# Kernel tuning notes

Hardware: AMD Instinct MI355X
Metric: run time of the kernel (lower is better)

The kernel has to match this reference:

```python
import jax, jax.numpy as jnp
import numpy as np

N = 100000      # nodes
E = 1600000     # edges (avg degree 16)
DIM = 128
HEADS = 8
HEAD_DIM = DIM // HEADS


def setup_inputs() -> dict:
    key = jax.random.key(0)
    k = jax.random.split(key, 6)
    stdv = 1.0 / np.sqrt(HEAD_DIM)  # init scale from reset_parameters
    x = jax.random.normal(k[0], (N, DIM), dtype=jnp.float32)
    edge_index = jax.random.randint(k[1], (2, E), 0, N, dtype=jnp.int32)
    W = jax.random.uniform(k[2], (DIM, DIM), jnp.float32, -stdv, stdv)
    b_proj = jnp.zeros((DIM,), jnp.float32)
    att_src = jax.random.uniform(k[3], (1, HEADS, HEAD_DIM), jnp.float32, -stdv, stdv)
    att_dst = jax.random.uniform(k[4], (1, HEADS, HEAD_DIM), jnp.float32, -stdv, stdv)
    bias = jnp.zeros((DIM,), jnp.float32)
    return {"x": x, "edge_index": edge_index, "W": W, "b_proj": b_proj,
            "att_src": att_src, "att_dst": att_dst, "bias": bias}


def reference(x, edge_index, W, b_proj, att_src, att_dst, bias):
    n = x.shape[0]
    # project, split heads: [N, H, Hd]
    xh = (x @ W.T + b_proj).reshape(n, HEADS, HEAD_DIM)
    # add_remaining_self_loops (random edges assumed loop-free)
    loops = jnp.arange(n, dtype=edge_index.dtype)
    src = jnp.concatenate([edge_index[0], loops])  # x_j index
    dst = jnp.concatenate([edge_index[1], loops])  # aggregation index
    # per-node attention logits [N, H]
    a_src = jnp.einsum('nhd,hd->nh', xh, att_src[0])
    a_dst = jnp.einsum('nhd,hd->nh', xh, att_dst[0])
    # per-edge score [Etot, H]
    alpha = jax.nn.leaky_relu(a_src[src] + a_dst[dst], negative_slope=0.2)
    # segment softmax over edges grouped by destination (self loops => no empty segments)
    mx = jax.ops.segment_max(alpha, dst, num_segments=n)
    ex = jnp.exp(alpha - mx[dst])
    denom = jax.ops.segment_sum(ex, dst, num_segments=n)
    alpha = ex / denom[dst]
    # message = alpha * x_j, scatter-add to destination
    msg = alpha[:, :, None] * xh[src]                      # [Etot, H, Hd]
    out = jax.ops.segment_sum(msg, dst, num_segments=n)    # [N, H, Hd]
    return out.reshape(n, DIM) + bias
```

## Files before the change

### kernel.cpp

```cpp
#include <hip/hip_runtime.h>
#include <hip/hip_bf16.h>

typedef __hip_bfloat16 bf16;
typedef __hip_bfloat162 bf162;
typedef __attribute__((ext_vector_type(8))) short short8;
typedef __attribute__((ext_vector_type(4))) float f32x4;

#define NN 100000
#define NE 1600000
#define ETOT (NE + NN)
#define DIM 128
#define HEADS 8

#define BSH 9
#define NBUK ((NN + 511) >> BSH)
#define EPB 2048
#define B1 ((ETOT + EPB - 1) / EPB)
#define MAXPER 40
#define PROJ_BLKS ((NN + 63) / 64)

__device__ __forceinline__ float lrelu(float v) { return v > 0.f ? v : 0.2f * v; }

__device__ __forceinline__ float load1(const void* p, int i, int isbf) {
    return isbf ? __bfloat162float(((const bf16*)p)[i]) : ((const float*)p)[i];
}
__device__ __forceinline__ float2 load2(const void* p, size_t pairIdx, int isbf) {
    if (isbf) return __bfloat1622float2(((const bf162*)p)[pairIdx]);
    return ((const float2*)p)[pairIdx];
}
__device__ __forceinline__ short f2bf(float f) {
    bf16 h = __float2bfloat16(f);
    return *reinterpret_cast<short*>(&h);
}

__global__ __launch_bounds__(256) void aug_kernel(
    const void* __restrict__ W, const void* __restrict__ bproj,
    const void* __restrict__ atts, const void* __restrict__ attd,
    int* __restrict__ flag, bf16* __restrict__ waug, float* __restrict__ wc)
{
    __shared__ bf16 Wl[128 * 128];
    __shared__ float av[256];
    __shared__ float red[256];
    const int tid = threadIdx.x;

    {
        const bf16* wb = (const bf16*)W;
        float m = 0.f;
        for (int i = tid; i < 8192; i += 256) {
            float v = fabsf(__bfloat162float(wb[i]));
            if (!(v < 1e30f)) v = 1e30f;
            m = fmaxf(m, v);
        }
        red[tid] = m;
        __syncthreads();
        for (int s = 128; s > 0; s >>= 1) {
            if (tid < s) red[tid] = fmaxf(red[tid], red[tid + s]);
            __syncthreads();
        }
    }
    const int isbf = (red[0] < 1.0f) ? 1 : 0;
    if (tid == 0) *flag = isbf;

    for (int i = tid; i < 2048; i += 256) {
        short8 v;
        if (isbf) {
            v = ((const short8*)W)[i];
        } else {
            const float* wp = (const float*)W + (size_t)i * 8;
            #pragma unroll
            for (int j = 0; j < 8; ++j) v[j] = f2bf(wp[j]);
        }
        ((short8*)Wl)[i] = v;
    }
    av[tid & 255] = (tid < 128) ? load1(atts, tid, isbf)
                                : load1(attd, tid - 128, isbf);
    __syncthreads();

    #pragma unroll
    for (int it = 0; it < 8; ++it) {
        const int o = tid + it * 256;
        const int row = o >> 7, col = o & 127;
        const int h = row & 7;
        const int ao = (row < 8) ? 0 : 128;
        float s = 0.f;
        #pragma unroll
        for (int t = 0; t < 16; ++t)
            s += av[ao + h * 16 + t] * __bfloat162float(Wl[(h * 16 + t) * 128 + col]);
        waug[o] = __float2bfloat16(s);
    }
    if (tid < 16) {
        const int h = tid & 7;
        const int ao = (tid < 8) ? 0 : 128;
        float s = 0.f;
        #pragma unroll
        for (int t = 0; t < 16; ++t)
            s += load1(bproj, h * 16 + t, isbf) * av[ao + h * 16 + t];
        wc[tid] = s;
    }
}

__global__ __launch_bounds__(256) void projcount_kernel(
    const void* __restrict__ x, const void* __restrict__ W,
    const void* __restrict__ bproj, const bf16* __restrict__ waug,
    const float* __restrict__ wc, const int* __restrict__ flag,
    bf16* __restrict__ xh, float* __restrict__ asrc, float* __restrict__ adst,
    const int* __restrict__ ei, int* __restrict__ cntmat)
{
    __shared__ short8 Wf[2304];
    __shared__ float bsh[DIM], csh[16];

    const int tid = threadIdx.x;

    if (blockIdx.x >= PROJ_BLKS) {
        const int b = blockIdx.x - PROJ_BLKS;
        int* cnt = (int*)Wf;
        for (int i = tid; i < NBUK; i += 256) cnt[i] = 0;
        __syncthreads();
        const int base = b * EPB;
        #pragma unroll
        for (int it = 0; it < EPB / 1024; ++it) {
            const int e = base + it * 1024 + tid * 4;
            if (e < ETOT) {
                int4 d4;
                if (e < NE) {
                    d4 = *(const int4*)(ei + NE + e);
                } else {
                    d4.x = e - NE; d4.y = d4.x + 1; d4.z = d4.x + 2; d4.w = d4.x + 3;
                }
                atomicAdd(&cnt[d4.x >> BSH], 1);
                atomicAdd(&cnt[d4.y >> BSH], 1);
                atomicAdd(&cnt[d4.z >> BSH], 1);
                atomicAdd(&cnt[d4.w >> BSH], 1);
            }
        }
        __syncthreads();
        for (int k = tid; k < NBUK; k += 256) cntmat[k * B1 + b] = cnt[k];
        return;
    }

    const int isbf = *flag;

    for (int c = tid; c < 2048; c += 256) {
        int j = c >> 4, kc = c & 15;
        int kb = kc >> 2, quad = kc & 3;
        int lane = quad * 16 + (j & 15);
        int jt = j >> 4;
        short8 v;
        if (isbf) {
            v = ((const short8*)W)[c];
        } else {
            const float* wp = (const float*)W + (size_t)j * DIM + kc * 8;
            #pragma unroll
            for (int i = 0; i < 8; ++i) v[i] = f2bf(wp[i]);
        }
        Wf[(jt * 4 + kb) * 64 + lane] = v;
    }
    {
        int c = tid;
        if (c < 256) {
            int j2 = c >> 4, kc = c & 15;
            int kb = kc >> 2, quad = kc & 3;
            Wf[(32 + kb) * 64 + quad * 16 + j2] = ((const short8*)waug)[c];
        }
    }
    if (tid < DIM) bsh[tid] = load1(bproj, tid, isbf);
    if (tid < 16)  csh[tid] = wc[tid];
    __syncthreads();

    const int w = tid >> 6;
    const int l = tid & 63;
    const int quad = l >> 4, mr = l & 15;
    const int n0 = blockIdx.x * 64 + w * 16;
    const int nArd = min(n0 + mr, NN - 1);

    short8 afr[4];
    if (isbf) {
        const short8* xp = (const short8*)x + (size_t)nArd * 16;
        #pragma unroll
        for (int kb = 0; kb < 4; ++kb) afr[kb] = xp[kb * 4 + quad];
    } else {
        const float* xp = (const float*)x + (size_t)nArd * DIM;
        #pragma unroll
        for (int kb = 0; kb < 4; ++kb) {
            const float* cp = xp + kb * 32 + quad * 8;
            float4 c0 = *(const float4*)cp;
            float4 c1 = *(const float4*)(cp + 4);
            short8 v;
            v[0] = f2bf(c0.x); v[1] = f2bf(c0.y); v[2] = f2bf(c0.z); v[3] = f2bf(c0.w);
            v[4] = f2bf(c1.x); v[5] = f2bf(c1.y); v[6] = f2bf(c1.z); v[7] = f2bf(c1.w);
            afr[kb] = v;
        }
    }

    f32x4 accs[8];
    #pragma unroll
    for (int jt = 0; jt < 8; ++jt) {
        f32x4 acc = {0.f, 0.f, 0.f, 0.f};
        #pragma unroll
        for (int kb = 0; kb < 4; ++kb) {
            short8 b = Wf[(jt * 4 + kb) * 64 + l];
            acc = __builtin_amdgcn_mfma_f32_16x16x32_bf16(afr[kb], b, acc, 0, 0, 0);
        }
        accs[jt] = acc;
    }
    f32x4 acca = {0.f, 0.f, 0.f, 0.f};
    #pragma unroll
    for (int kb = 0; kb < 4; ++kb) {
        short8 b = Wf[(32 + kb) * 64 + l];
        acca = __builtin_amdgcn_mfma_f32_16x16x32_bf16(afr[kb], b, acca, 0, 0, 0);
    }

    __syncthreads();

    bf16* sw = ((bf16*)Wf) + w * (16 * 136);
    #pragma unroll
    for (int jt = 0; jt < 8; ++jt) {
        const int jj = jt * 16 + mr;
        const float bv = bsh[jj];
        #pragma unroll
        for (int r = 0; r < 4; ++r)
            sw[(quad * 4 + r) * 136 + jj] = __float2bfloat16(accs[jt][r] + bv);
    }
    #pragma unroll
    for (int g = 0; g < 4; ++g) {
        const int row = g * 4 + (l >> 4);
        const int n = n0 + row;
        if (n < NN)
            *((short8*)(xh + (size_t)n * DIM) + (l & 15)) =
                *(const short8*)(sw + row * 136 + (l & 15) * 8);
    }

    {
        const float cst = csh[mr];
        #pragma unroll
        for (int r = 0; r < 4; ++r) {
            const int n = n0 + quad * 4 + r;
            if (n < NN) {
                float v = acca[r] + cst;
                if (mr < 8) asrc[n * HEADS + mr] = v;
                else        adst[n * HEADS + (mr - 8)] = v;
            }
        }
    }
}

__global__ __launch_bounds__(256) void csr_colscan_kernel(const int* __restrict__ cntmat,
                                                          int* __restrict__ cntpre,
                                                          int* __restrict__ btot)
{
    const int k = blockIdx.x, t = threadIdx.x;
    int v[4];
    int s = 0;
    #pragma unroll
    for (int j = 0; j < 4; ++j) {
        const int c = t * 4 + j;
        v[j] = (c < B1) ? cntmat[k * B1 + c] : 0;
        s += v[j];
    }
    const int l = t & 63, w = t >> 6;
    int inc = s;
    #pragma unroll
    for (int off = 1; off < 64; off <<= 1) {
        int u = __shfl_up(inc, off);
        if (l >= off) inc += u;
    }
    __shared__ int wt[4];
    if (l == 63) wt[w] = inc;
    __syncthreads();
    int add = 0;
    #pragma unroll
    for (int i = 0; i < 4; ++i) if (i < w) add += wt[i];
    int run = add + inc - s;
    #pragma unroll
    for (int j = 0; j < 4; ++j) {
        const int c = t * 4 + j;
        if (c < B1) cntpre[k * B1 + c] = run;
        run += v[j];
    }
    if (t == 255) btot[k] = add + inc;
}

__device__ __forceinline__ void scan_btot(const int* __restrict__ btot,
                                          int* __restrict__ bb, int* __restrict__ wt4)
{
    const int t = threadIdx.x;
    const int v = (t < NBUK) ? btot[t] : 0;
    const int l = t & 63, w = t >> 6;
    int inc = v;
    #pragma unroll
    for (int off = 1; off < 64; off <<= 1) {
        int u = __shfl_up(inc, off);
        if (l >= off) inc += u;
    }
    if (l == 63) wt4[w] = inc;
    __syncthreads();
    int add = 0;
    #pragma unroll
    for (int i = 0; i < 4; ++i) if (i < w) add += wt4[i];
    if (t < NBUK) bb[t] = add + inc - v;
    __syncthreads();
}

__global__ __launch_bounds__(256) void csr_scatter_kernel(const int* __restrict__ ei,
                                                          const int* __restrict__ cntpre,
                                                          const int* __restrict__ btot,
                                                          int* __restrict__ esrc)
{
    __shared__ int cur[NBUK];
    __shared__ int bb[NBUK];
    __shared__ int wt4[4];
    const int t = threadIdx.x, b = blockIdx.x;

    scan_btot(btot, bb, wt4);
    for (int k = t; k < NBUK; k += 256) cur[k] = bb[k] + cntpre[k * B1 + b];
    __syncthreads();

    const int base = b * EPB;
    #pragma unroll
    for (int it = 0; it < EPB / 1024; ++it) {
        const int e = base + it * 1024 + t * 4;
        if (e < ETOT) {
            int4 d4, s4;
            if (e < NE) {
                s4 = *(const int4*)(ei + e);
                d4 = *(const int4*)(ei + NE + e);
            } else {
                s4.x = e - NE; s4.y = s4.x + 1; s4.z = s4.x + 2; s4.w = s4.x + 3;
                d4 = s4;
            }
            const int p0 = atomicAdd(&cur[d4.x >> BSH], 1);
            const int p1 = atomicAdd(&cur[d4.y >> BSH], 1);
            const int p2 = atomicAdd(&cur[d4.z >> BSH], 1);
            const int p3 = atomicAdd(&cur[d4.w >> BSH], 1);
            esrc[p0] = s4.x | ((d4.x & 511) << 17);
            esrc[p1] = s4.y | ((d4.y & 511) << 17);
            esrc[p2] = s4.z | ((d4.z & 511) << 17);
            esrc[p3] = s4.w | ((d4.w & 511) << 17);
        }
    }
}

__global__ __launch_bounds__(256) void csr_bucket_kernel(const int* __restrict__ btot,
                                                         int* __restrict__ esrc,
                                                         int* __restrict__ rowstart)
{
    __shared__ int hist[512];
    __shared__ int pre[512];
    __shared__ int bb[NBUK];
    __shared__ int wt4[4];
    const int k = blockIdx.x, t = threadIdx.x;

    scan_btot(btot, bb, wt4);
    const int start = bb[k];
    const int end = start + btot[k];
    if (k == 0 && t == 0) rowstart[NN] = ETOT;

    hist[t] = 0;
    hist[t + 256] = 0;
    __syncthreads();

    int v[MAXPER];
    #pragma unroll
    for (int j = 0; j < MAXPER; ++j) {
        const int idx = start + j * 256 + t;
        v[j] = (idx < end) ? esrc[idx] : -1;
    }
    #pragma unroll
    for (int j = 0; j < MAXPER; ++j)
        if (v[j] >= 0) atomicAdd(&hist[(v[j] >> 17) & 511], 1);
    __syncthreads();

    const int h0 = hist[2 * t], h1 = hist[2 * t + 1];
    const int pv = h0 + h1;
    const int l = t & 63, w = t >> 6;
    int inc = pv;
    #pragma unroll
    for (int off = 1; off < 64; off <<= 1) {
        int u = __shfl_up(inc, off);
        if (l >= off) inc += u;
    }
    if (l == 63) wt4[w] = inc;
    __syncthreads();
    int add = 0;
    #pragma unroll
    for (int i = 0; i < 4; ++i) if (i < w) add += wt4[i];
    const int ex = add + inc - pv;
    pre[2 * t] = ex;
    pre[2 * t + 1] = ex + h0;

    const int d0 = (k << BSH) + 2 * t;
    if (d0 < NN)     rowstart[d0]     = start + ex;
    if (d0 + 1 < NN) rowstart[d0 + 1] = start + ex + h0;
    __syncthreads();

    #pragma unroll
    for (int j = 0; j < MAXPER; ++j) {
        if (v[j] >= 0) {
            const int pos = atomicAdd(&pre[(v[j] >> 17) & 511], 1);
            esrc[start + pos] = v[j] & 0x1FFFF;
        }
    }
}

__global__ __launch_bounds__(256) void gather_kernel(
    const int* __restrict__ rowstart, const int* __restrict__ esrc,
    const float* __restrict__ asrc, const float* __restrict__ adst,
    const bf16* __restrict__ xh, const void* __restrict__ bias,
    const int* __restrict__ flag, void* __restrict__ out)
{
    const int d = blockIdx.x * 4 + (threadIdx.x >> 6);
    if (d >= NN) return;
    const int l = threadIdx.x & 63;
    const int h = l >> 3;
    const int isbf = *flag;

    const float ad = adst[d * HEADS + h];
    const int r0 = rowstart[d], r1 = rowstart[d + 1];
    const bf162* __restrict__ xrow = (const bf162*)xh;
    float a0 = 0.f, a1 = 0.f, ds = 0.f;

    int p = r0;
    for (; p + 8 <= r1; p += 8) {
        int s[8];
        #pragma unroll
        for (int j = 0; j < 8; ++j) s[j] = esrc[p + j];
        float v[8];
        #pragma unroll
        for (int j = 0; j < 8; ++j) v[j] = asrc[(unsigned)s[j] * HEADS + h];
        float2 xv[8];
        #pragma unroll
        for (int j = 0; j < 8; ++j)
            xv[j] = __bfloat1622float2(xrow[(unsigned)s[j] * 64u + (unsigned)l]);
        #pragma unroll
        for (int j = 0; j < 8; ++j) {
            float wj = __expf(lrelu(v[j] + ad));
            a0 += wj * xv[j].x;
            a1 += wj * xv[j].y;
            ds += wj;
        }
    }
    for (; p + 4 <= r1; p += 4) {
        int s0 = esrc[p + 0], s1 = esrc[p + 1], s2 = esrc[p + 2], s3 = esrc[p + 3];
        float v0 = asrc[(unsigned)s0 * HEADS + h];
        float v1 = asrc[(unsigned)s1 * HEADS + h];
        float v2 = asrc[(unsigned)s2 * HEADS + h];
        float v3 = asrc[(unsigned)s3 * HEADS + h];
        float2 x0 = __bfloat1622float2(xrow[(unsigned)s0 * 64u + (unsigned)l]);
        float2 x1 = __bfloat1622float2(xrow[(unsigned)s1 * 64u + (unsigned)l]);
        float2 x2 = __bfloat1622float2(xrow[(unsigned)s2 * 64u + (unsigned)l]);
        float2 x3 = __bfloat1622float2(xrow[(unsigned)s3 * 64u + (unsigned)l]);
        float w0 = __expf(lrelu(v0 + ad));
        float w1 = __expf(lrelu(v1 + ad));
        float w2 = __expf(lrelu(v2 + ad));
        float w3 = __expf(lrelu(v3 + ad));
        a0 += w0 * x0.x + w1 * x1.x + w2 * x2.x + w3 * x3.x;
        a1 += w0 * x0.y + w1 * x1.y + w2 * x2.y + w3 * x3.y;
        ds += (w0 + w1) + (w2 + w3);
    }
    for (; p < r1; ++p) {
        int s = esrc[p];
        float w = __expf(lrelu(asrc[(unsigned)s * HEADS + h] + ad));
        float2 xf = __bfloat1622float2(xrow[(unsigned)s * 64u + (unsigned)l]);
        a0 += w * xf.x;
        a1 += w * xf.y;
        ds += w;
    }

    float inv = 1.f / ds;
    float2 bf = load2(bias, l, isbf);
    float o0 = a0 * inv + bf.x;
    float o1 = a1 * inv + bf.y;
    if (isbf) {
        bf162 o;
        o.x = __float2bfloat16(o0);
        o.y = __float2bfloat16(o1);
        ((bf162*)out)[(size_t)d * 64 + l] = o;
    } else {
        ((float2*)out)[(size_t)d * 64 + l] = make_float2(o0, o1);
    }
}

extern "C" void kernel_launch(void* const* d_in, const int* in_sizes, int n_in,
                              void* d_out, int out_size, void* d_ws, size_t ws_size,
                              hipStream_t stream)
{
    const void* x     = d_in[0];
    const int*  ei    = (const int*)d_in[1];
    const void* W     = d_in[2];
    const void* bproj = d_in[3];
    const void* atts  = d_in[4];
    const void* attd  = d_in[5];
    const void* bias  = d_in[6];

    char* p = (char*)d_ws;
    int*    flag     = (int*)p;    p += 16;
    bf16*   xh       = (bf16*)p;   p += (size_t)NN * DIM * sizeof(bf16);
    float*  asrc     = (float*)p;  p += (size_t)NN * HEADS * sizeof(float);
    float*  adst     = (float*)p;  p += (size_t)NN * HEADS * sizeof(float);
    int*    rowstart = (int*)p;    p += (size_t)(NN + 1) * sizeof(int) + 12;
    int*    esrc     = (int*)p;    p += (size_t)ETOT * sizeof(int);
    int*    cntmat   = (int*)p;    p += (size_t)NBUK * B1 * sizeof(int);
    int*    cntpre   = (int*)p;    p += (size_t)NBUK * B1 * sizeof(int);
    int*    btot     = (int*)p;    p += ((NBUK + 3) & ~3) * sizeof(int);
    bf16*   waug     = (bf16*)p;   p += 16 * 128 * sizeof(bf16);
    float*  wc       = (float*)p;  p += 16 * sizeof(float);

    aug_kernel<<<1, 256, 0, stream>>>(W, bproj, atts, attd, flag, waug, wc);
    projcount_kernel<<<PROJ_BLKS + B1, 256, 0, stream>>>(x, W, bproj, waug, wc,
                                                         flag, xh, asrc, adst,
                                                         ei, cntmat);
    csr_colscan_kernel<<<NBUK, 256, 0, stream>>>(cntmat, cntpre, btot);
    csr_scatter_kernel<<<B1, 256, 0, stream>>>(ei, cntpre, btot, esrc);
    csr_bucket_kernel<<<NBUK, 256, 0, stream>>>(btot, esrc, rowstart);
    gather_kernel<<<(NN + 3) / 4, 256, 0, stream>>>(rowstart, esrc, asrc, adst,
                                                    xh, bias, flag, d_out);
}
```

Baseline: 274.9 us.

## Replace per-block count matrix and column scan with global atomic bucket offsets

The bucket-count pass now accumulates per-bucket totals straight into a global array with atomics, and it runs inside the weight-augmentation launch. The scatter blocks, fused with projection, each claim a contiguous slice within each bucket through a global atomic cursor, so the count-matrix write, the column-scan kernel and a separate scatter launch all go away. This cuts two kernel launches and a round trip through the count matrix. In exchange, the order of edges within a bucket is no longer deterministic, and a memset is added to clear the counters.

```diff
diff --git a/kernel.cpp b/kernel.cpp
--- a/kernel.cpp
+++ b/kernel.cpp
@@ -16,6 +16,8 @@
 #define NBUK ((NN + 511) >> BSH)
 #define EPB 2048
 #define B1 ((ETOT + EPB - 1) / EPB)
+#define EPB2 8192
+#define B2 ((ETOT + EPB2 - 1) / EPB2)
 #define MAXPER 40
 #define PROJ_BLKS ((NN + 63) / 64)
 
@@ -33,92 +35,43 @@
     return *reinterpret_cast<short*>(&h);
 }
 
-__global__ __launch_bounds__(256) void aug_kernel(
+__device__ __forceinline__ void scan_btot(const int* __restrict__ btot,
+                                          int* __restrict__ bb, int* __restrict__ wt4)
+{
+    const int t = threadIdx.x;
+    const int v = (t < NBUK) ? btot[t] : 0;
+    const int l = t & 63, w = t >> 6;
+    int inc = v;
+    #pragma unroll
+    for (int off = 1; off < 64; off <<= 1) {
+        int u = __shfl_up(inc, off);
+        if (l >= off) inc += u;
+    }
+    if (l == 63) wt4[w] = inc;
+    __syncthreads();
+    int add = 0;
+    #pragma unroll
+    for (int i = 0; i < 4; ++i) if (i < w) add += wt4[i];
+    if (t < NBUK) bb[t] = add + inc - v;
+    __syncthreads();
+}
+
+__global__ __launch_bounds__(256) void aug_count_kernel(
     const void* __restrict__ W, const void* __restrict__ bproj,
     const void* __restrict__ atts, const void* __restrict__ attd,
-    int* __restrict__ flag, bf16* __restrict__ waug, float* __restrict__ wc)
+    int* __restrict__ flag, bf16* __restrict__ waug, float* __restrict__ wc,
+    const int* __restrict__ ei, int* __restrict__ btot)
 {
-    __shared__ bf16 Wl[128 * 128];
-    __shared__ float av[256];
-    __shared__ float red[256];
+    __shared__ char smem[32768 + 2048];
     const int tid = threadIdx.x;
 
-    {
-        const bf16* wb = (const bf16*)W;
-        float m = 0.f;
-        for (int i = tid; i < 8192; i += 256) {
-            float v = fabsf(__bfloat162float(wb[i]));
-            if (!(v < 1e30f)) v = 1e30f;
-            m = fmaxf(m, v);
-        }
-        red[tid] = m;
-        __syncthreads();
-        for (int s = 128; s > 0; s >>= 1) {
-            if (tid < s) red[tid] = fmaxf(red[tid], red[tid + s]);
-            __syncthreads();
-        }
-    }
-    const int isbf = (red[0] < 1.0f) ? 1 : 0;
-    if (tid == 0) *flag = isbf;
-
-    for (int i = tid; i < 2048; i += 256) {
-        short8 v;
-        if (isbf) {
-            v = ((const short8*)W)[i];
-        } else {
-            const float* wp = (const float*)W + (size_t)i * 8;
-            #pragma unroll
-            for (int j = 0; j < 8; ++j) v[j] = f2bf(wp[j]);
-        }
-        ((short8*)Wl)[i] = v;
-    }
-    av[tid & 255] = (tid < 128) ? load1(atts, tid, isbf)
-                                : load1(attd, tid - 128, isbf);
-    __syncthreads();
-
-    #pragma unroll
-    for (int it = 0; it < 8; ++it) {
-        const int o = tid + it * 256;
-        const int row = o >> 7, col = o & 127;
-        const int h = row & 7;
-        const int ao = (row < 8) ? 0 : 128;
-        float s = 0.f;
-        #pragma unroll
-        for (int t = 0; t < 16; ++t)
-            s += av[ao + h * 16 + t] * __bfloat162float(Wl[(h * 16 + t) * 128 + col]);
-        waug[o] = __float2bfloat16(s);
-    }
-    if (tid < 16) {
-        const int h = tid & 7;
-        const int ao = (tid < 8) ? 0 : 128;
-        float s = 0.f;
-        #pragma unroll
-        for (int t = 0; t < 16; ++t)
-            s += load1(bproj, h * 16 + t, isbf) * av[ao + h * 16 + t];
-        wc[tid] = s;
-    }
-}
-
-__global__ __launch_bounds__(256) void projcount_kernel(
-    const void* __restrict__ x, const void* __restrict__ W,
-    const void* __restrict__ bproj, const bf16* __restrict__ waug,
-    const float* __restrict__ wc, const int* __restrict__ flag,
-    bf16* __restrict__ xh, float* __restrict__ asrc, float* __restrict__ adst,
-    const int* __restrict__ ei, int* __restrict__ cntmat)
-{
-    __shared__ short8 Wf[2304];
-    __shared__ float bsh[DIM], csh[16];
-
-    const int tid = threadIdx.x;
-
-    if (blockIdx.x >= PROJ_BLKS) {
-        const int b = blockIdx.x - PROJ_BLKS;
-        int* cnt = (int*)Wf;
+    if (blockIdx.x < B2) {
+        int* cnt = (int*)smem;
         for (int i = tid; i < NBUK; i += 256) cnt[i] = 0;
         __syncthreads();
-        const int base = b * EPB;
-        #pragma unroll
-        for (int it = 0; it < EPB / 1024; ++it) {
+        const int base = blockIdx.x * EPB2;
+        #pragma unroll
+        for (int it = 0; it < EPB2 / 1024; ++it) {
             const int e = base + it * 1024 + tid * 4;
             if (e < ETOT) {
                 int4 d4;
@@ -134,7 +87,141 @@
             }
         }
         __syncthreads();
-        for (int k = tid; k < NBUK; k += 256) cntmat[k * B1 + b] = cnt[k];
+        for (int k = tid; k < NBUK; k += 256) {
+            const int c = cnt[k];
+            if (c) atomicAdd(&btot[k], c);
+        }
+        return;
+    }
+
+    bf16*  Wl  = (bf16*)smem;
+    float* av  = (float*)(smem + 32768);
+    float* red = av + 256;
+
+    {
+        const bf16* wb = (const bf16*)W;
+        float m = 0.f;
+        for (int i = tid; i < 8192; i += 256) {
+            float v = fabsf(__bfloat162float(wb[i]));
+            if (!(v < 1e30f)) v = 1e30f;
+            m = fmaxf(m, v);
+        }
+        red[tid] = m;
+        __syncthreads();
+        for (int s = 128; s > 0; s >>= 1) {
+            if (tid < s) red[tid] = fmaxf(red[tid], red[tid + s]);
+            __syncthreads();
+        }
+    }
+    const int isbf = (red[0] < 1.0f) ? 1 : 0;
+    if (tid == 0) *flag = isbf;
+
+    for (int i = tid; i < 2048; i += 256) {
+        short8 v;
+        if (isbf) {
+            v = ((const short8*)W)[i];
+        } else {
+            const float* wp = (const float*)W + (size_t)i * 8;
+            #pragma unroll
+            for (int j = 0; j < 8; ++j) v[j] = f2bf(wp[j]);
+        }
+        ((short8*)Wl)[i] = v;
+    }
+    av[tid & 255] = (tid < 128) ? load1(atts, tid, isbf)
+                                : load1(attd, tid - 128, isbf);
+    __syncthreads();
+
+    #pragma unroll
+    for (int it = 0; it < 8; ++it) {
+        const int o = tid + it * 256;
+        const int row = o >> 7, col = o & 127;
+        const int h = row & 7;
+        const int ao = (row < 8) ? 0 : 128;
+        float s = 0.f;
+        #pragma unroll
+        for (int t = 0; t < 16; ++t)
+            s += av[ao + h * 16 + t] * __bfloat162float(Wl[(h * 16 + t) * 128 + col]);
+        waug[o] = __float2bfloat16(s);
+    }
+    if (tid < 16) {
+        const int h = tid & 7;
+        const int ao = (tid < 8) ? 0 : 128;
+        float s = 0.f;
+        #pragma unroll
+        for (int t = 0; t < 16; ++t)
+            s += load1(bproj, h * 16 + t, isbf) * av[ao + h * 16 + t];
+        wc[tid] = s;
+    }
+}
+
+__global__ __launch_bounds__(256) void proj_scatter_kernel(
+    const void* __restrict__ x, const void* __restrict__ W,
+    const void* __restrict__ bproj, const bf16* __restrict__ waug,
+    const float* __restrict__ wc, const int* __restrict__ flag,
+    bf16* __restrict__ xh, float* __restrict__ asrc, float* __restrict__ adst,
+    const int* __restrict__ ei, const int* __restrict__ btot,
+    int* __restrict__ gcur, int* __restrict__ esrc)
+{
+    __shared__ short8 Wf[2304];
+    __shared__ float bsh[DIM], csh[16];
+
+    const int tid = threadIdx.x;
+
+    if (blockIdx.x >= PROJ_BLKS) {
+        int* hist = (int*)Wf;
+        int* cur  = hist + NBUK;
+        int* bb   = cur + NBUK;
+        int* wt4  = bb + NBUK;
+        const int b = blockIdx.x - PROJ_BLKS;
+
+        for (int i = tid; i < NBUK; i += 256) hist[i] = 0;
+        __syncthreads();
+
+        const int base = b * EPB;
+        int4 s4[2], d4[2];
+        int valid[2];
+        #pragma unroll
+        for (int it = 0; it < 2; ++it) {
+            const int e = base + it * 1024 + tid * 4;
+            valid[it] = (e < ETOT);
+            if (valid[it]) {
+                if (e < NE) {
+                    s4[it] = *(const int4*)(ei + e);
+                    d4[it] = *(const int4*)(ei + NE + e);
+                } else {
+                    s4[it].x = e - NE; s4[it].y = s4[it].x + 1;
+                    s4[it].z = s4[it].x + 2; s4[it].w = s4[it].x + 3;
+                    d4[it] = s4[it];
+                }
+                atomicAdd(&hist[d4[it].x >> BSH], 1);
+                atomicAdd(&hist[d4[it].y >> BSH], 1);
+                atomicAdd(&hist[d4[it].z >> BSH], 1);
+                atomicAdd(&hist[d4[it].w >> BSH], 1);
+            }
+        }
+        __syncthreads();
+
+        scan_btot(btot, bb, wt4);
+
+        for (int k = tid; k < NBUK; k += 256) {
+            const int c = hist[k];
+            cur[k] = c ? (bb[k] + atomicAdd(&gcur[k], c)) : 0;
+        }
+        __syncthreads();
+
+        #pragma unroll
+        for (int it = 0; it < 2; ++it) {
+            if (valid[it]) {
+                const int p0 = atomicAdd(&cur[d4[it].x >> BSH], 1);
+                const int p1 = atomicAdd(&cur[d4[it].y >> BSH], 1);
+                const int p2 = atomicAdd(&cur[d4[it].z >> BSH], 1);
+                const int p3 = atomicAdd(&cur[d4[it].w >> BSH], 1);
+                esrc[p0] = s4[it].x | ((d4[it].x & 511) << 17);
+                esrc[p1] = s4[it].y | ((d4[it].y & 511) << 17);
+                esrc[p2] = s4[it].z | ((d4[it].z & 511) << 17);
+                esrc[p3] = s4[it].w | ((d4[it].w & 511) << 17);
+            }
+        }
         return;
     }
 
@@ -240,102 +327,6 @@
                 if (mr < 8) asrc[n * HEADS + mr] = v;
                 else        adst[n * HEADS + (mr - 8)] = v;
             }
-        }
-    }
-}
-
-__global__ __launch_bounds__(256) void csr_colscan_kernel(const int* __restrict__ cntmat,
-                                                          int* __restrict__ cntpre,
-                                                          int* __restrict__ btot)
-{
-    const int k = blockIdx.x, t = threadIdx.x;
-    int v[4];
-    int s = 0;
-    #pragma unroll
-    for (int j = 0; j < 4; ++j) {
-        const int c = t * 4 + j;
-        v[j] = (c < B1) ? cntmat[k * B1 + c] : 0;
-        s += v[j];
-    }
-    const int l = t & 63, w = t >> 6;
-    int inc = s;
-    #pragma unroll
-    for (int off = 1; off < 64; off <<= 1) {
-        int u = __shfl_up(inc, off);
-        if (l >= off) inc += u;
-    }
-    __shared__ int wt[4];
-    if (l == 63) wt[w] = inc;
-    __syncthreads();
-    int add = 0;
-    #pragma unroll
-    for (int i = 0; i < 4; ++i) if (i < w) add += wt[i];
-    int run = add + inc - s;
-    #pragma unroll
-    for (int j = 0; j < 4; ++j) {
-        const int c = t * 4 + j;
-        if (c < B1) cntpre[k * B1 + c] = run;
-        run += v[j];
-    }
-    if (t == 255) btot[k] = add + inc;
-}
-
-__device__ __forceinline__ void scan_btot(const int* __restrict__ btot,
-                                          int* __restrict__ bb, int* __restrict__ wt4)
-{
-    const int t = threadIdx.x;
-    const int v = (t < NBUK) ? btot[t] : 0;
-    const int l = t & 63, w = t >> 6;
-    int inc = v;
-    #pragma unroll
-    for (int off = 1; off < 64; off <<= 1) {
-        int u = __shfl_up(inc, off);
-        if (l >= off) inc += u;
-    }
-    if (l == 63) wt4[w] = inc;
-    __syncthreads();
-    int add = 0;
-    #pragma unroll
-    for (int i = 0; i < 4; ++i) if (i < w) add += wt4[i];
-    if (t < NBUK) bb[t] = add + inc - v;
-    __syncthreads();
-}
-
-__global__ __launch_bounds__(256) void csr_scatter_kernel(const int* __restrict__ ei,
-                                                          const int* __restrict__ cntpre,
-                                                          const int* __restrict__ btot,
-                                                          int* __restrict__ esrc)
-{
-    __shared__ int cur[NBUK];
-    __shared__ int bb[NBUK];
-    __shared__ int wt4[4];
-    const int t = threadIdx.x, b = blockIdx.x;
-
-    scan_btot(btot, bb, wt4);
-    for (int k = t; k < NBUK; k += 256) cur[k] = bb[k] + cntpre[k * B1 + b];
-    __syncthreads();
-
-    const int base = b * EPB;
-    #pragma unroll
-    for (int it = 0; it < EPB / 1024; ++it) {
-        const int e = base + it * 1024 + t * 4;
-        if (e < ETOT) {
-            int4 d4, s4;
-            if (e < NE) {
-                s4 = *(const int4*)(ei + e);
-                d4 = *(const int4*)(ei + NE + e);
-            } else {
-                s4.x = e - NE; s4.y = s4.x + 1; s4.z = s4.x + 2; s4.w = s4.x + 3;
-                d4 = s4;
-            }
-            const int p0 = atomicAdd(&cur[d4.x >> BSH], 1);
-            const int p1 = atomicAdd(&cur[d4.y >> BSH], 1);
-            const int p2 = atomicAdd(&cur[d4.z >> BSH], 1);
-            const int p3 = atomicAdd(&cur[d4.w >> BSH], 1);
-            esrc[p0] = s4.x | ((d4.x & 511) << 17);
-            esrc[p1] = s4.y | ((d4.y & 511) << 17);
-            esrc[p2] = s4.z | ((d4.z & 511) << 17);
-            esrc[p3] = s4.w | ((d4.w & 511) << 17);
         }
     }
 }
@@ -499,18 +490,18 @@
     float*  adst     = (float*)p;  p += (size_t)NN * HEADS * sizeof(float);
     int*    rowstart = (int*)p;    p += (size_t)(NN + 1) * sizeof(int) + 12;
     int*    esrc     = (int*)p;    p += (size_t)ETOT * sizeof(int);
-    int*    cntmat   = (int*)p;    p += (size_t)NBUK * B1 * sizeof(int);
-    int*    cntpre   = (int*)p;    p += (size_t)NBUK * B1 * sizeof(int);
-    int*    btot     = (int*)p;    p += ((NBUK + 3) & ~3) * sizeof(int);
+    int*    btot     = (int*)p;    p += 256 * sizeof(int);
+    int*    gcur     = (int*)p;    p += 256 * sizeof(int);
     bf16*   waug     = (bf16*)p;   p += 16 * 128 * sizeof(bf16);
     float*  wc       = (float*)p;  p += 16 * sizeof(float);
 
-    aug_kernel<<<1, 256, 0, stream>>>(W, bproj, atts, attd, flag, waug, wc);
-    projcount_kernel<<<PROJ_BLKS + B1, 256, 0, stream>>>(x, W, bproj, waug, wc,
-                                                         flag, xh, asrc, adst,
-                                                         ei, cntmat);
-    csr_colscan_kernel<<<NBUK, 256, 0, stream>>>(cntmat, cntpre, btot);
-    csr_scatter_kernel<<<B1, 256, 0, stream>>>(ei, cntpre, btot, esrc);
+    hipMemsetAsync(btot, 0, 512 * sizeof(int), stream);
+
+    aug_count_kernel<<<B2 + 1, 256, 0, stream>>>(W, bproj, atts, attd, flag,
+                                                 waug, wc, ei, btot);
+    proj_scatter_kernel<<<PROJ_BLKS + B1, 256, 0, stream>>>(x, W, bproj, waug, wc,
+                                                            flag, xh, asrc, adst,
+                                                            ei, btot, gcur, esrc);
     csr_bucket_kernel<<<NBUK, 256, 0, stream>>>(btot, esrc, rowstart);
     gather_kernel<<<(NN + 3) / 4, 256, 0, stream>>>(rowstart, esrc, asrc, adst,
                                                     xh, bias, flag, d_out);
```

After: 273.8 us. About the same (-0.4%).
